# Optimization experiments

Measured on AMD Instinct MI355X. Metric: run time of the kernel, lower is better.

The kernel has to match this reference:

```python
import jax, jax.numpy as jnp
import numpy as np

VOCAB, EMBED, HIDDEN, LAYERS = 128, 512, 1024, 2
BATCH, SEQ = 64, 512


def _lstm_layer(x, w_ih, w_hh, b_ih, b_hh):
    # x: [B, T, In]; w_ih: [4H, In]; w_hh: [4H, H]
    B, T, _ = x.shape
    H = w_hh.shape[1]
    # Precompute the input contribution for all timesteps at once: [B, T, 4H]
    xin = jnp.einsum('bti,gi->btg', x, w_ih) + b_ih + b_hh

    def step(carry, xt):
        h, c = carry
        z = xt + h @ w_hh.T                      # [B, 4H]
        i, f, g, o = jnp.split(z, 4, axis=-1)    # PyTorch gate order i,f,g,o
        i = jax.nn.sigmoid(i)
        f = jax.nn.sigmoid(f)
        g = jnp.tanh(g)
        o = jax.nn.sigmoid(o)
        c = f * c + i * g
        h = o * jnp.tanh(c)
        return (h, c), h

    h0 = jnp.zeros((B, H), x.dtype)
    c0 = jnp.zeros((B, H), x.dtype)
    _, hs = jax.lax.scan(step, (h0, c0), jnp.swapaxes(xin, 0, 1))  # [T, B, H]
    return jnp.swapaxes(hs, 0, 1)                                   # [B, T, H]


def setup_inputs() -> dict:
    key = jax.random.key(0)
    ks = jax.random.split(key, 12)
    s_e = 1.0 / np.sqrt(EMBED)
    s_h = 1.0 / np.sqrt(HIDDEN)
    return {
        'x': jax.random.randint(ks[0], (BATCH, SEQ), 0, VOCAB, dtype=jnp.int32),
        'embedding': jax.random.normal(ks[1], (VOCAB, EMBED), jnp.float32),
        'w_ih_0': jax.random.normal(ks[2], (4 * HIDDEN, EMBED), jnp.float32) * s_e,
        'w_hh_0': jax.random.normal(ks[3], (4 * HIDDEN, HIDDEN), jnp.float32) * s_h,
        'b_ih_0': jax.random.normal(ks[4], (4 * HIDDEN,), jnp.float32) * s_h,
        'b_hh_0': jax.random.normal(ks[5], (4 * HIDDEN,), jnp.float32) * s_h,
        'w_ih_1': jax.random.normal(ks[6], (4 * HIDDEN, HIDDEN), jnp.float32) * s_h,
        'w_hh_1': jax.random.normal(ks[7], (4 * HIDDEN, HIDDEN), jnp.float32) * s_h,
        'b_ih_1': jax.random.normal(ks[8], (4 * HIDDEN,), jnp.float32) * s_h,
        'b_hh_1': jax.random.normal(ks[9], (4 * HIDDEN,), jnp.float32) * s_h,
        'fc_w': jax.random.normal(ks[10], (VOCAB, HIDDEN), jnp.float32) * s_h,
        'fc_b': jax.random.normal(ks[11], (VOCAB,), jnp.float32) * s_h,
    }


def reference(x, embedding, w_ih_0, w_hh_0, b_ih_0, b_hh_0,
              w_ih_1, w_hh_1, b_ih_1, b_hh_1, fc_w, fc_b):
    emb = embedding[x]                                   # [B, T, E]
    h1 = _lstm_layer(emb, w_ih_0, w_hh_0, b_ih_0, b_hh_0)  # [B, T, H]
    h2 = _lstm_layer(h1, w_ih_1, w_hh_1, b_ih_1, b_hh_1)   # [B, T, H]
    return h2 @ fc_w.T + fc_b                            # [B, T, V]
```

## Files before the change

kernel.cpp:

```cpp
#include <hip/hip_runtime.h>


typedef _Float16 v8h __attribute__((ext_vector_type(8)));
typedef float v4f __attribute__((ext_vector_type(4)));
typedef _Float16 h2v __attribute__((ext_vector_type(2)));
typedef unsigned long long u64t;

__device__ __forceinline__ float sigf(float x) {
  return 1.0f / (1.0f + __expf(-x));
}
__device__ __forceinline__ float tanhfast(float x) {
  return 1.0f - 2.0f / (1.0f + __expf(2.0f * x));
}

__global__ __launch_bounds__(256) void prep_kernel(
    const float* __restrict__ emb, const float* __restrict__ w_ih0,
    const float* __restrict__ b_ih0, const float* __restrict__ b_hh0,
    const float* __restrict__ fc_w, _Float16* __restrict__ tableV,
    _Float16* __restrict__ fcwT, unsigned* __restrict__ zbuf,
    unsigned* __restrict__ bar) {
  const int blk = blockIdx.x, tid = threadIdx.x;
  if (blk < 2048) {
    const int C = blk * 2 + (tid >> 7);
    const int v = tid & 127;
    const int row =
        ((C >> 2) & 3) * 1024 + (C >> 5) * 8 + ((C >> 4) & 1) * 4 + (C & 3);
    const float* er = emb + v * 512;
    const float* wr = w_ih0 + row * 512;
    float a0 = 0.f, a1 = 0.f, a2 = 0.f, a3 = 0.f;
#pragma unroll 4
    for (int k = 0; k < 512; k += 4) {
      a0 = fmaf(er[k], wr[k], a0);
      a1 = fmaf(er[k + 1], wr[k + 1], a1);
      a2 = fmaf(er[k + 2], wr[k + 2], a2);
      a3 = fmaf(er[k + 3], wr[k + 3], a3);
    }
    tableV[v * 4096 + C] =
        (_Float16)(b_ih0[row] + b_hh0[row] + ((a0 + a1) + (a2 + a3)));
  } else if (blk < 2560) {
    const int idx = (blk - 2048) * 256 + tid;
    const int v = idx & 127, k = idx >> 7;
    fcwT[k * 128 + v] = (_Float16)fc_w[v * 1024 + k];
  } else if (blk < 2592) {
    const int idx = (blk - 2560) * 256 + tid;
#pragma unroll
    for (int q = 0; q < 16; ++q) zbuf[idx * 16 + q] = 0u;
  } else {
    for (int i = tid; i < 512; i += 256) bar[i] = 0u;
  }
}

__global__ __launch_bounds__(512, 1) void lstm_mfma(
    const int* __restrict__ x, const _Float16* __restrict__ tableV,
    const float* __restrict__ w_hh0, const float* __restrict__ w_ih1,
    const float* __restrict__ w_hh1, const float* __restrict__ b_ih1,
    const float* __restrict__ b_hh1, _Float16* __restrict__ hseq,
    unsigned* __restrict__ bar) {
  __shared__ __align__(16) float zs[8 * 4 * 8 * 64];

  const int tid = threadIdx.x, blk = blockIdx.x;
  const bool isL1 = blk >= 128;
  const int sub = isL1 ? blk - 128 : blk;
  const int xcd = sub & 7, bidx = sub >> 3;
  const int m = bidx >> 3, cg2 = xcd * 8 + (bidx & 7);
  const int w = tid >> 6, l = tid & 63;
  const int lane16 = l & 15, quad = l >> 4;
  const int g = lane16 >> 2, jj = lane16 & 3;
  const int colp = jj * 4 + g;

  const int b = w * 4 + quad;
  const int uu = lane16;
  const int bg = m * 32 + b;
  const int ubase = (isL1 ? 1024 : 0) + cg2 * 16;
  const int colo = ((uu >> 2) * 16 + (uu & 3) * 4) ^ ((w & 1) << 4);

  float cst = 0.0f;

  if (!isL1) {
    v8h bf[4][4];
#pragma unroll
    for (int ct = 0; ct < 4; ++ct) {
      const int row = g * 1024 + cg2 * 16 + ct * 4 + jj;
      const float* rp = w_hh0 + row * 1024 + w * 128 + quad * 8;
#pragma unroll
      for (int kk = 0; kk < 4; ++kk) {
        const float4 f0 = *(const float4*)(rp + kk * 32);
        const float4 f1 = *(const float4*)(rp + kk * 32 + 4);
        v8h bb;
        bb[0] = (_Float16)f0.x; bb[1] = (_Float16)f0.y;
        bb[2] = (_Float16)f0.z; bb[3] = (_Float16)f0.w;
        bb[4] = (_Float16)f1.x; bb[5] = (_Float16)f1.y;
        bb[6] = (_Float16)f1.z; bb[7] = (_Float16)f1.w;
        bf[ct][kk] = bb;
      }
    }
    const int Cbase = (cg2 * 2 + (uu >> 3)) * 32 + ((uu >> 2) & 1) * 16 + (uu & 3);
    _Float16 tvh[4];
    {
      const int xv = x[bg * 512];
#pragma unroll
      for (int gg = 0; gg < 4; ++gg)
        tvh[gg] = tableV[xv * 4096 + Cbase + gg * 4];
    }
    unsigned* arr = &bar[(m * 8 + xcd) * 16];
    const unsigned* pw = &bar[(m * 8) * 16];

    for (int it = 0; it < 512; ++it) {
      if (tid == 0 && it > 0) {
        const unsigned tgt = 8u * (unsigned)it;
        for (;;) {
          unsigned mn = 0xffffffffu;
#pragma unroll
          for (int gg = 0; gg < 8; ++gg) {
            const unsigned vv = __hip_atomic_load(
                pw + gg * 16, __ATOMIC_RELAXED, __HIP_MEMORY_SCOPE_AGENT);
            mn = vv < mn ? vv : mn;
          }
          if (mn >= tgt) break;
          __builtin_amdgcn_s_sleep(1);
        }
      }
      __syncthreads();
      asm volatile("" ::: "memory");
      const _Float16* hr = hseq + (size_t)it * 131072;
      _Float16* hw = hseq + (size_t)(it + 1) * 131072;

      const _Float16* a0p = hr + (m * 32 + lane16) * 2048 + w * 128 + quad * 8;
      const _Float16* a1p = a0p + 16 * 2048;
      v8h A0[4], A1[4];
#pragma unroll
      for (int kk = 0; kk < 4; ++kk) A0[kk] = *(const v8h*)(a0p + kk * 32);
#pragma unroll
      for (int kk = 0; kk < 4; ++kk) A1[kk] = *(const v8h*)(a1p + kk * 32);
      v4f ac0[4] = {{0, 0, 0, 0}, {0, 0, 0, 0}, {0, 0, 0, 0}, {0, 0, 0, 0}};
      v4f ac1[4] = {{0, 0, 0, 0}, {0, 0, 0, 0}, {0, 0, 0, 0}, {0, 0, 0, 0}};
#pragma unroll
      for (int kk = 0; kk < 4; ++kk)
#pragma unroll
        for (int ct = 0; ct < 4; ++ct) {
          ac0[ct] = __builtin_amdgcn_mfma_f32_16x16x32_f16(A0[kk], bf[ct][kk], ac0[ct], 0, 0, 0);
          ac1[ct] = __builtin_amdgcn_mfma_f32_16x16x32_f16(A1[kk], bf[ct][kk], ac1[ct], 0, 0, 0);
        }

#pragma unroll
      for (int r = 0; r < 4; ++r)
#pragma unroll
        for (int ct = 0; ct < 4; ++ct) {
          const int col = (ct * 16 + colp) ^ ((quad & 1) << 4);
          zs[((w * 4 + r) * 8 + quad) * 64 + col] = ac0[ct][r];
          zs[((w * 4 + r) * 8 + 4 + quad) * 64 + col] = ac1[ct][r];
        }
      __syncthreads();

      v4f z;
      z[0] = (float)tvh[0]; z[1] = (float)tvh[1];
      z[2] = (float)tvh[2]; z[3] = (float)tvh[3];
#pragma unroll
      for (int wv = 0; wv < 8; ++wv)
        z += *(const v4f*)&zs[((wv * 4 + quad) * 8 + w) * 64 + colo];
      const float ig = sigf(z[0]), fg = sigf(z[1]);
      const float gg2 = tanhfast(z[2]), og = sigf(z[3]);
      cst = fg * cst + ig * gg2;
      const float hv = og * tanhfast(cst);

      const unsigned hu =
          (unsigned)__builtin_bit_cast(unsigned short, (_Float16)hv);
      const unsigned p1 = (unsigned)__shfl_xor((int)hu, 1, 64);
      const unsigned lo = (l & 1) ? ((p1 & 0xffffu) | (hu << 16))
                                  : ((hu & 0xffffu) | (p1 << 16));
      const unsigned p2 = (unsigned)__shfl_xor((int)lo, 2, 64);
      if ((l & 3) == 0) {
        const u64t val = (u64t)lo | ((u64t)p2 << 32);
        __hip_atomic_store((u64t*)(hw + bg * 2048 + ubase + (l & 15)), val,
                           __ATOMIC_RELAXED, __HIP_MEMORY_SCOPE_AGENT);
      }
      if (it + 1 < 512) {
        const int xv = x[bg * 512 + it + 1];
#pragma unroll
        for (int gg = 0; gg < 4; ++gg)
          tvh[gg] = tableV[xv * 4096 + Cbase + gg * 4];
      }
      asm volatile("s_waitcnt vmcnt(0)" ::: "memory");
      __syncthreads();
      if (tid == 0) atomicAdd(arr, 1u);
    }
  } else {
    v8h bf[4][8];
    {
      const float* Wsrc = (w < 4) ? w_ih1 : w_hh1;
      const int kbase = (w < 4) ? w * 256 : w * 256 - 1024;
#pragma unroll
      for (int ct = 0; ct < 4; ++ct) {
        const int row = g * 1024 + cg2 * 16 + ct * 4 + jj;
        const float* rp = Wsrc + row * 1024 + kbase + quad * 8;
#pragma unroll
        for (int kk = 0; kk < 8; ++kk) {
          const float4 f0 = *(const float4*)(rp + kk * 32);
          const float4 f1 = *(const float4*)(rp + kk * 32 + 4);
          v8h bb;
          bb[0] = (_Float16)f0.x; bb[1] = (_Float16)f0.y;
          bb[2] = (_Float16)f0.z; bb[3] = (_Float16)f0.w;
          bb[4] = (_Float16)f1.x; bb[5] = (_Float16)f1.y;
          bb[6] = (_Float16)f1.z; bb[7] = (_Float16)f1.w;
          bf[ct][kk] = bb;
        }
      }
    }
    v4f bias4;
#pragma unroll
    for (int gg = 0; gg < 4; ++gg) {
      const int row = gg * 1024 + cg2 * 16 + uu;
      bias4[gg] = b_ih1[row] + b_hh1[row];
    }
    unsigned* arr = &bar[((2 + m) * 8 + xcd) * 16];
    const unsigned* pw0 = &bar[(m * 8) * 16];
    const unsigned* pw1 = &bar[((2 + m) * 8) * 16];

    for (int it = 1; it <= 512; ++it) {
      if (tid == 0) {
        const unsigned t0 = 8u * (unsigned)it;
        const unsigned t1 = 8u * (unsigned)(it - 1);
        for (;;) {
          unsigned mn0 = 0xffffffffu, mn1 = 0xffffffffu;
#pragma unroll
          for (int gg = 0; gg < 8; ++gg) {
            const unsigned v0 = __hip_atomic_load(
                pw0 + gg * 16, __ATOMIC_RELAXED, __HIP_MEMORY_SCOPE_AGENT);
            const unsigned v1 = __hip_atomic_load(
                pw1 + gg * 16, __ATOMIC_RELAXED, __HIP_MEMORY_SCOPE_AGENT);
            mn0 = v0 < mn0 ? v0 : mn0;
            mn1 = v1 < mn1 ? v1 : mn1;
          }
          if (mn0 >= t0 && mn1 >= t1) break;
          __builtin_amdgcn_s_sleep(1);
        }
      }
      __syncthreads();
      asm volatile("" ::: "memory");
      const _Float16* hr = hseq + (size_t)it * 131072;
      _Float16* hw = hseq + (size_t)(it + 1) * 131072;

      const _Float16* a0p = hr + (m * 32 + lane16) * 2048 + w * 256 + quad * 8;
      const _Float16* a1p = a0p + 16 * 2048;
      v8h A0[8], A1[8];
#pragma unroll
      for (int kk = 0; kk < 8; ++kk) A0[kk] = *(const v8h*)(a0p + kk * 32);
#pragma unroll
      for (int kk = 0; kk < 8; ++kk) A1[kk] = *(const v8h*)(a1p + kk * 32);
      v4f ac0[4] = {{0, 0, 0, 0}, {0, 0, 0, 0}, {0, 0, 0, 0}, {0, 0, 0, 0}};
      v4f ac1[4] = {{0, 0, 0, 0}, {0, 0, 0, 0}, {0, 0, 0, 0}, {0, 0, 0, 0}};
#pragma unroll
      for (int kk = 0; kk < 8; ++kk)
#pragma unroll
        for (int ct = 0; ct < 4; ++ct) {
          ac0[ct] = __builtin_amdgcn_mfma_f32_16x16x32_f16(A0[kk], bf[ct][kk], ac0[ct], 0, 0, 0);
          ac1[ct] = __builtin_amdgcn_mfma_f32_16x16x32_f16(A1[kk], bf[ct][kk], ac1[ct], 0, 0, 0);
        }

#pragma unroll
      for (int r = 0; r < 4; ++r)
#pragma unroll
        for (int ct = 0; ct < 4; ++ct) {
          const int col = (ct * 16 + colp) ^ ((quad & 1) << 4);
          zs[((w * 4 + r) * 8 + quad) * 64 + col] = ac0[ct][r];
          zs[((w * 4 + r) * 8 + 4 + quad) * 64 + col] = ac1[ct][r];
        }
      __syncthreads();

      v4f z = bias4;
#pragma unroll
      for (int wv = 0; wv < 8; ++wv)
        z += *(const v4f*)&zs[((wv * 4 + quad) * 8 + w) * 64 + colo];
      const float ig = sigf(z[0]), fg = sigf(z[1]);
      const float gg2 = tanhfast(z[2]), og = sigf(z[3]);
      cst = fg * cst + ig * gg2;
      const float hv = og * tanhfast(cst);

      const unsigned hu =
          (unsigned)__builtin_bit_cast(unsigned short, (_Float16)hv);
      const unsigned p1 = (unsigned)__shfl_xor((int)hu, 1, 64);
      const unsigned lo = (l & 1) ? ((p1 & 0xffffu) | (hu << 16))
                                  : ((hu & 0xffffu) | (p1 << 16));
      const unsigned p2 = (unsigned)__shfl_xor((int)lo, 2, 64);
      if ((l & 3) == 0) {
        const u64t val = (u64t)lo | ((u64t)p2 << 32);
        __hip_atomic_store((u64t*)(hw + bg * 2048 + ubase + (l & 15)), val,
                           __ATOMIC_RELAXED, __HIP_MEMORY_SCOPE_AGENT);
      }
      asm volatile("s_waitcnt vmcnt(0)" ::: "memory");
      __syncthreads();
      if (tid == 0) atomicAdd(arr, 1u);
    }
  }
}

__global__ __launch_bounds__(256, 2) void fc_kernel(
    const _Float16* __restrict__ hseq, const _Float16* __restrict__ fcwT,
    const float* __restrict__ fc_b, float* __restrict__ out) {
  __shared__ float hl[16][1024];
  const int tid = threadIdx.x;
  const int t = blockIdx.x >> 2, bs = blockIdx.x & 3;
  const int v = tid & 127, hh = tid >> 7;

  const h2v* hp = (const h2v*)hseq;
  const size_t base = (size_t)(t + 2) * 65536 + 512;
  for (int idx = tid; idx < 8192; idx += 256) {
    const int bl = idx >> 9, kp = idx & 511;
    const h2v pr = hp[base + (size_t)((bs * 16 + bl)) * 1024 + kp];
    hl[bl][2 * kp] = (float)pr.x;
    hl[bl][2 * kp + 1] = (float)pr.y;
  }
  __syncthreads();

  float acc[8];
#pragma unroll
  for (int i = 0; i < 8; ++i) acc[i] = 0.0f;
  const int bl0 = hh * 8;
#pragma unroll 1
  for (int k4 = 0; k4 < 256; ++k4) {
    const int k = k4 * 4;
    const float w0 = (float)fcwT[(k + 0) * 128 + v];
    const float w1 = (float)fcwT[(k + 1) * 128 + v];
    const float w2 = (float)fcwT[(k + 2) * 128 + v];
    const float w3 = (float)fcwT[(k + 3) * 128 + v];
#pragma unroll
    for (int i = 0; i < 8; ++i) {
      const float4 hv = *(const float4*)&hl[bl0 + i][k];
      acc[i] += hv.x * w0 + hv.y * w1 + hv.z * w2 + hv.w * w3;
    }
  }
  const float bias = fc_b[v];
#pragma unroll
  for (int i = 0; i < 8; ++i) {
    const int bb = bs * 16 + bl0 + i;
    out[(bb * 512 + t) * 128 + v] = acc[i] + bias;
  }
}

extern "C" void kernel_launch(void* const* d_in, const int* in_sizes, int n_in,
                              void* d_out, int out_size, void* d_ws,
                              size_t ws_size, hipStream_t stream) {
  const int* x = (const int*)d_in[0];
  const float* emb = (const float*)d_in[1];
  const float* w_ih0 = (const float*)d_in[2];
  const float* w_hh0 = (const float*)d_in[3];
  const float* b_ih0 = (const float*)d_in[4];
  const float* b_hh0 = (const float*)d_in[5];
  const float* w_ih1 = (const float*)d_in[6];
  const float* w_hh1 = (const float*)d_in[7];
  const float* b_ih1 = (const float*)d_in[8];
  const float* b_hh1 = (const float*)d_in[9];
  const float* fc_w = (const float*)d_in[10];
  const float* fc_b = (const float*)d_in[11];
  float* out = (float*)d_out;

  char* ws = (char*)d_ws;
  _Float16* tableV = (_Float16*)(ws);
  _Float16* fcwT = (_Float16*)(ws + 1048576);
  unsigned* bar = (unsigned*)(ws + 1310720);
  _Float16* hseq = (_Float16*)(ws + 1376256);
  unsigned* zb = (unsigned*)(ws + 1376256);

  prep_kernel<<<2593, 256, 0, stream>>>(emb, w_ih0, b_ih0, b_hh0, fc_w,
                                        tableV, fcwT, zb, bar);

  const _Float16* tableVc = tableV;
  _Float16* hseqa = hseq;
  unsigned* bara = bar;
  void* args[] = {(void*)&x,     (void*)&tableVc, (void*)&w_hh0,
                  (void*)&w_ih1, (void*)&w_hh1,   (void*)&b_ih1,
                  (void*)&b_hh1, (void*)&hseqa,   (void*)&bara};
  hipLaunchCooperativeKernel(lstm_mfma, dim3(256), dim3(512), args, 0, stream);

  fc_kernel<<<2048, 256, 0, stream>>>(hseq, fcwT, fc_b, out);
}
```

Measured before the change: 3.967 ms.

## Move layer-1 input projection into layer-0 blocks via ring buffer

Layer-0 blocks now also multiply their fresh h_t by w_ih1 and write the layer-1 input contribution into a 16-slot global ring buffer. This halves the per-step K dimension and MFMA count on the layer-1 critical path. Layer 0 runs one extra iteration and waits on layer-1 progress so it cannot overwrite unread ring slots. The cost is doubled MFMA work and more shared memory in layer-0 blocks, an extra global round trip, and tighter coupling between the two layers' barriers.

```diff
diff --git a/kernel.cpp b/kernel.cpp
--- a/kernel.cpp
+++ b/kernel.cpp
@@ -55,8 +55,9 @@
     const float* __restrict__ w_hh0, const float* __restrict__ w_ih1,
     const float* __restrict__ w_hh1, const float* __restrict__ b_ih1,
     const float* __restrict__ b_hh1, _Float16* __restrict__ hseq,
-    unsigned* __restrict__ bar) {
+    float* __restrict__ xin1r, unsigned* __restrict__ bar) {
   __shared__ __align__(16) float zs[8 * 4 * 8 * 64];
+  __shared__ __align__(16) float zs2[8 * 4 * 8 * 64];
 
   const int tid = threadIdx.x, blk = blockIdx.x;
   const bool isL1 = blk >= 128;
@@ -77,21 +78,29 @@
   float cst = 0.0f;
 
   if (!isL1) {
-    v8h bf[4][4];
+    v8h bfh[4][4], bfi[4][4];
 #pragma unroll
     for (int ct = 0; ct < 4; ++ct) {
       const int row = g * 1024 + cg2 * 16 + ct * 4 + jj;
-      const float* rp = w_hh0 + row * 1024 + w * 128 + quad * 8;
+      const float* rph = w_hh0 + row * 1024 + w * 128 + quad * 8;
+      const float* rpi = w_ih1 + row * 1024 + w * 128 + quad * 8;
 #pragma unroll
       for (int kk = 0; kk < 4; ++kk) {
-        const float4 f0 = *(const float4*)(rp + kk * 32);
-        const float4 f1 = *(const float4*)(rp + kk * 32 + 4);
-        v8h bb;
-        bb[0] = (_Float16)f0.x; bb[1] = (_Float16)f0.y;
-        bb[2] = (_Float16)f0.z; bb[3] = (_Float16)f0.w;
-        bb[4] = (_Float16)f1.x; bb[5] = (_Float16)f1.y;
-        bb[6] = (_Float16)f1.z; bb[7] = (_Float16)f1.w;
-        bf[ct][kk] = bb;
+        const float4 h0 = *(const float4*)(rph + kk * 32);
+        const float4 h1 = *(const float4*)(rph + kk * 32 + 4);
+        const float4 i0 = *(const float4*)(rpi + kk * 32);
+        const float4 i1 = *(const float4*)(rpi + kk * 32 + 4);
+        v8h bh, bi;
+        bh[0] = (_Float16)h0.x; bh[1] = (_Float16)h0.y;
+        bh[2] = (_Float16)h0.z; bh[3] = (_Float16)h0.w;
+        bh[4] = (_Float16)h1.x; bh[5] = (_Float16)h1.y;
+        bh[6] = (_Float16)h1.z; bh[7] = (_Float16)h1.w;
+        bi[0] = (_Float16)i0.x; bi[1] = (_Float16)i0.y;
+        bi[2] = (_Float16)i0.z; bi[3] = (_Float16)i0.w;
+        bi[4] = (_Float16)i1.x; bi[5] = (_Float16)i1.y;
+        bi[6] = (_Float16)i1.z; bi[7] = (_Float16)i1.w;
+        bfh[ct][kk] = bh;
+        bfi[ct][kk] = bi;
       }
     }
     const int Cbase = (cg2 * 2 + (uu >> 3)) * 32 + ((uu >> 2) & 1) * 16 + (uu & 3);
@@ -103,20 +112,25 @@
         tvh[gg] = tableV[xv * 4096 + Cbase + gg * 4];
     }
     unsigned* arr = &bar[(m * 8 + xcd) * 16];
-    const unsigned* pw = &bar[(m * 8) * 16];
-
-    for (int it = 0; it < 512; ++it) {
+    const unsigned* pw0 = &bar[(m * 8) * 16];
+    const unsigned* pw1 = &bar[((2 + m) * 8) * 16];
+
+    for (int it = 0; it <= 512; ++it) {
       if (tid == 0 && it > 0) {
-        const unsigned tgt = 8u * (unsigned)it;
+        const unsigned tgt0 = 8u * (unsigned)it;
+        const unsigned tgt1 = (it >= 17) ? 8u * (unsigned)(it - 16) : 0u;
         for (;;) {
-          unsigned mn = 0xffffffffu;
+          unsigned mn0 = 0xffffffffu, mn1 = 0xffffffffu;
 #pragma unroll
           for (int gg = 0; gg < 8; ++gg) {
-            const unsigned vv = __hip_atomic_load(
-                pw + gg * 16, __ATOMIC_RELAXED, __HIP_MEMORY_SCOPE_AGENT);
-            mn = vv < mn ? vv : mn;
+            const unsigned v0 = __hip_atomic_load(
+                pw0 + gg * 16, __ATOMIC_RELAXED, __HIP_MEMORY_SCOPE_AGENT);
+            const unsigned v1 = __hip_atomic_load(
+                pw1 + gg * 16, __ATOMIC_RELAXED, __HIP_MEMORY_SCOPE_AGENT);
+            mn0 = v0 < mn0 ? v0 : mn0;
+            mn1 = v1 < mn1 ? v1 : mn1;
           }
-          if (mn >= tgt) break;
+          if (mn0 >= tgt0 && mn1 >= tgt1) break;
           __builtin_amdgcn_s_sleep(1);
         }
       }
@@ -134,12 +148,16 @@
       for (int kk = 0; kk < 4; ++kk) A1[kk] = *(const v8h*)(a1p + kk * 32);
       v4f ac0[4] = {{0, 0, 0, 0}, {0, 0, 0, 0}, {0, 0, 0, 0}, {0, 0, 0, 0}};
       v4f ac1[4] = {{0, 0, 0, 0}, {0, 0, 0, 0}, {0, 0, 0, 0}, {0, 0, 0, 0}};
+      v4f bc0[4] = {{0, 0, 0, 0}, {0, 0, 0, 0}, {0, 0, 0, 0}, {0, 0, 0, 0}};
+      v4f bc1[4] = {{0, 0, 0, 0}, {0, 0, 0, 0}, {0, 0, 0, 0}, {0, 0, 0, 0}};
 #pragma unroll
       for (int kk = 0; kk < 4; ++kk)
 #pragma unroll
         for (int ct = 0; ct < 4; ++ct) {
-          ac0[ct] = __builtin_amdgcn_mfma_f32_16x16x32_f16(A0[kk], bf[ct][kk], ac0[ct], 0, 0, 0);
-          ac1[ct] = __builtin_amdgcn_mfma_f32_16x16x32_f16(A1[kk], bf[ct][kk], ac1[ct], 0, 0, 0);
+          ac0[ct] = __builtin_amdgcn_mfma_f32_16x16x32_f16(A0[kk], bfh[ct][kk], ac0[ct], 0, 0, 0);
+          ac1[ct] = __builtin_amdgcn_mfma_f32_16x16x32_f16(A1[kk], bfh[ct][kk], ac1[ct], 0, 0, 0);
+          bc0[ct] = __builtin_amdgcn_mfma_f32_16x16x32_f16(A0[kk], bfi[ct][kk], bc0[ct], 0, 0, 0);
+          bc1[ct] = __builtin_amdgcn_mfma_f32_16x16x32_f16(A1[kk], bfi[ct][kk], bc1[ct], 0, 0, 0);
         }
 
 #pragma unroll
@@ -149,6 +167,8 @@
           const int col = (ct * 16 + colp) ^ ((quad & 1) << 4);
           zs[((w * 4 + r) * 8 + quad) * 64 + col] = ac0[ct][r];
           zs[((w * 4 + r) * 8 + 4 + quad) * 64 + col] = ac1[ct][r];
+          zs2[((w * 4 + r) * 8 + quad) * 64 + col] = bc0[ct][r];
+          zs2[((w * 4 + r) * 8 + 4 + quad) * 64 + col] = bc1[ct][r];
         }
       __syncthreads();
 
@@ -174,6 +194,21 @@
         __hip_atomic_store((u64t*)(hw + bg * 2048 + ubase + (l & 15)), val,
                            __ATOMIC_RELAXED, __HIP_MEMORY_SCOPE_AGENT);
       }
+
+      v4f z2 = {0.f, 0.f, 0.f, 0.f};
+#pragma unroll
+      for (int wv = 0; wv < 8; ++wv)
+        z2 += *(const v4f*)&zs2[((wv * 4 + quad) * 8 + w) * 64 + colo];
+      {
+        u64t* xp = (u64t*)&xin1r[((((size_t)(it & 15) * 64 + bg) * 64 + cg2)
+                                  << 6) + uu * 4];
+        const ulonglong2 qq = __builtin_bit_cast(ulonglong2, z2);
+        __hip_atomic_store(xp, qq.x, __ATOMIC_RELAXED,
+                           __HIP_MEMORY_SCOPE_AGENT);
+        __hip_atomic_store(xp + 1, qq.y, __ATOMIC_RELAXED,
+                           __HIP_MEMORY_SCOPE_AGENT);
+      }
+
       if (it + 1 < 512) {
         const int xv = x[bg * 512 + it + 1];
 #pragma unroll
@@ -185,25 +220,21 @@
       if (tid == 0) atomicAdd(arr, 1u);
     }
   } else {
-    v8h bf[4][8];
-    {
-      const float* Wsrc = (w < 4) ? w_ih1 : w_hh1;
-      const int kbase = (w < 4) ? w * 256 : w * 256 - 1024;
-#pragma unroll
-      for (int ct = 0; ct < 4; ++ct) {
-        const int row = g * 1024 + cg2 * 16 + ct * 4 + jj;
-        const float* rp = Wsrc + row * 1024 + kbase + quad * 8;
-#pragma unroll
-        for (int kk = 0; kk < 8; ++kk) {
-          const float4 f0 = *(const float4*)(rp + kk * 32);
-          const float4 f1 = *(const float4*)(rp + kk * 32 + 4);
-          v8h bb;
-          bb[0] = (_Float16)f0.x; bb[1] = (_Float16)f0.y;
-          bb[2] = (_Float16)f0.z; bb[3] = (_Float16)f0.w;
-          bb[4] = (_Float16)f1.x; bb[5] = (_Float16)f1.y;
-          bb[6] = (_Float16)f1.z; bb[7] = (_Float16)f1.w;
-          bf[ct][kk] = bb;
-        }
+    v8h bf[4][4];
+#pragma unroll
+    for (int ct = 0; ct < 4; ++ct) {
+      const int row = g * 1024 + cg2 * 16 + ct * 4 + jj;
+      const float* rp = w_hh1 + row * 1024 + w * 128 + quad * 8;
+#pragma unroll
+      for (int kk = 0; kk < 4; ++kk) {
+        const float4 f0 = *(const float4*)(rp + kk * 32);
+        const float4 f1 = *(const float4*)(rp + kk * 32 + 4);
+        v8h bb;
+        bb[0] = (_Float16)f0.x; bb[1] = (_Float16)f0.y;
+        bb[2] = (_Float16)f0.z; bb[3] = (_Float16)f0.w;
+        bb[4] = (_Float16)f1.x; bb[5] = (_Float16)f1.y;
+        bb[6] = (_Float16)f1.z; bb[7] = (_Float16)f1.w;
+        bf[ct][kk] = bb;
       }
     }
     v4f bias4;
@@ -218,7 +249,7 @@
 
     for (int it = 1; it <= 512; ++it) {
       if (tid == 0) {
-        const unsigned t0 = 8u * (unsigned)it;
+        const unsigned t0 = 8u * (unsigned)(it + 1);
         const unsigned t1 = 8u * (unsigned)(it - 1);
         for (;;) {
           unsigned mn0 = 0xffffffffu, mn1 = 0xffffffffu;
@@ -240,17 +271,25 @@
       const _Float16* hr = hseq + (size_t)it * 131072;
       _Float16* hw = hseq + (size_t)(it + 1) * 131072;
 
-      const _Float16* a0p = hr + (m * 32 + lane16) * 2048 + w * 256 + quad * 8;
+      const u64t* xp = (const u64t*)&xin1r[((((size_t)(it & 15) * 64 + bg) *
+                                            64 + cg2) << 6) + uu * 4];
+      const u64t xlo = __hip_atomic_load(xp, __ATOMIC_RELAXED,
+                                         __HIP_MEMORY_SCOPE_AGENT);
+      const u64t xhi = __hip_atomic_load(xp + 1, __ATOMIC_RELAXED,
+                                         __HIP_MEMORY_SCOPE_AGENT);
+
+      const _Float16* a0p =
+          hr + (m * 32 + lane16) * 2048 + 1024 + w * 128 + quad * 8;
       const _Float16* a1p = a0p + 16 * 2048;
-      v8h A0[8], A1[8];
-#pragma unroll
-      for (int kk = 0; kk < 8; ++kk) A0[kk] = *(const v8h*)(a0p + kk * 32);
-#pragma unroll
-      for (int kk = 0; kk < 8; ++kk) A1[kk] = *(const v8h*)(a1p + kk * 32);
+      v8h A0[4], A1[4];
+#pragma unroll
+      for (int kk = 0; kk < 4; ++kk) A0[kk] = *(const v8h*)(a0p + kk * 32);
+#pragma unroll
+      for (int kk = 0; kk < 4; ++kk) A1[kk] = *(const v8h*)(a1p + kk * 32);
       v4f ac0[4] = {{0, 0, 0, 0}, {0, 0, 0, 0}, {0, 0, 0, 0}, {0, 0, 0, 0}};
       v4f ac1[4] = {{0, 0, 0, 0}, {0, 0, 0, 0}, {0, 0, 0, 0}, {0, 0, 0, 0}};
 #pragma unroll
-      for (int kk = 0; kk < 8; ++kk)
+      for (int kk = 0; kk < 4; ++kk)
 #pragma unroll
         for (int ct = 0; ct < 4; ++ct) {
           ac0[ct] = __builtin_amdgcn_mfma_f32_16x16x32_f16(A0[kk], bf[ct][kk], ac0[ct], 0, 0, 0);
@@ -267,7 +306,10 @@
         }
       __syncthreads();
 
-      v4f z = bias4;
+      ulonglong2 xq;
+      xq.x = xlo;
+      xq.y = xhi;
+      v4f z = bias4 + __builtin_bit_cast(v4f, xq);
 #pragma unroll
       for (int wv = 0; wv < 8; ++wv)
         z += *(const v4f*)&zs[((wv * 4 + quad) * 8 + w) * 64 + colo];
@@ -359,6 +401,7 @@
   _Float16* fcwT = (_Float16*)(ws + 1048576);
   unsigned* bar = (unsigned*)(ws + 1310720);
   _Float16* hseq = (_Float16*)(ws + 1376256);
+  float* xin1r = (float*)(ws + 136118272);
   unsigned* zb = (unsigned*)(ws + 1376256);
 
   prep_kernel<<<2593, 256, 0, stream>>>(emb, w_ih0, b_ih0, b_hh0, fc_w,
@@ -366,10 +409,12 @@
 
   const _Float16* tableVc = tableV;
   _Float16* hseqa = hseq;
+  float* xin1ra = xin1r;
   unsigned* bara = bar;
   void* args[] = {(void*)&x,     (void*)&tableVc, (void*)&w_hh0,
                   (void*)&w_ih1, (void*)&w_hh1,   (void*)&b_ih1,
-                  (void*)&b_hh1, (void*)&hseqa,   (void*)&bara};
+                  (void*)&b_hh1, (void*)&hseqa,   (void*)&xin1ra,
+                  (void*)&bara};
   hipLaunchCooperativeKernel(lstm_mfma, dim3(256), dim3(512), args, 0, stream);
 
   fc_kernel<<<2048, 256, 0, stream>>>(hseq, fcwT, fc_b, out);
```

After: 4.076 ms. 1.03x slower.
